# Optimization experiments

Hardware: AMD Instinct MI355X
Metric: run time of the kernel (lower is better)

The kernel has to match this reference:

```python
import jax, jax.numpy as jnp
import numpy as np

N = 20000      # nodes
E = 160000     # edges (avg degree 16)
IN_DIM = 256
HID = 128      # hidden_dim == per-head out_channels in PyG TransformerConv
HEADS = 4
EPS = 1e-5


def setup_inputs() -> dict:
    key = jax.random.key(0)
    ks = jax.random.split(key, 24)

    def w(k, shape, scale=0.05):
        return jax.random.normal(k, shape, dtype=jnp.float32) * scale

    inp = {
        "x": jax.random.normal(ks[0], (N, IN_DIM), dtype=jnp.float32),
        "edge_index": jax.random.randint(ks[1], (2, E), 0, N, dtype=jnp.int32),
        # input projection
        "lin_w": w(ks[2], (IN_DIM, HID)), "lin_b": jnp.zeros((HID,), jnp.float32),
    }
    i = 3
    for l in (1, 2):
        inp[f"q_w{l}"] = w(ks[i], (HID, HEADS * HID)); i += 1
        inp[f"q_b{l}"] = jnp.zeros((HEADS * HID,), jnp.float32)
        inp[f"k_w{l}"] = w(ks[i], (HID, HEADS * HID)); i += 1
        inp[f"k_b{l}"] = jnp.zeros((HEADS * HID,), jnp.float32)
        inp[f"v_w{l}"] = w(ks[i], (HID, HEADS * HID)); i += 1
        inp[f"v_b{l}"] = jnp.zeros((HEADS * HID,), jnp.float32)
        inp[f"s_w{l}"] = w(ks[i], (HID, HID)); i += 1
        inp[f"s_b{l}"] = jnp.zeros((HID,), jnp.float32)
        inp[f"ln_g{l}"] = jnp.ones((HID,), jnp.float32)
        inp[f"ln_b{l}"] = jnp.zeros((HID,), jnp.float32)
    return inp


def _segment_softmax(scores, seg, num):
    # scores: [E, HEADS], seg: [E] destination indices
    m = jax.ops.segment_max(scores, seg, num_segments=num)
    m = jnp.where(jnp.isfinite(m), m, 0.0)  # guard empty segments
    e = jnp.exp(scores - m[seg])
    d = jax.ops.segment_sum(e, seg, num_segments=num)
    return e / (d[seg] + 1e-16)


def _transformer_conv(x, src, dst, qw, qb, kw, kb, vw, vb, sw, sb):
    # PyG TransformerConv(HID, HID, heads=HEADS, concat=False)
    n = x.shape[0]
    q = (x @ qw + qb).reshape(n, HEADS, HID)
    k = (x @ kw + kb).reshape(n, HEADS, HID)
    v = (x @ vw + vb).reshape(n, HEADS, HID)
    # per-edge attention: query at dst (i), key/value at src (j)
    alpha = jnp.einsum("ehd,ehd->eh", q[dst], k[src]) / jnp.sqrt(jnp.float32(HID))
    alpha = _segment_softmax(alpha, dst, n)                 # [E, HEADS]
    msg = v[src] * alpha[..., None]                          # [E, HEADS, HID]
    out = jax.ops.segment_sum(msg, dst, num_segments=n)      # [N, HEADS, HID]
    out = out.mean(axis=1)                                   # concat=False -> head mean
    return out + x @ sw + sb                                 # root skip connection


def _layer_norm(x, g, b):
    mu = x.mean(-1, keepdims=True)
    var = ((x - mu) ** 2).mean(-1, keepdims=True)
    return (x - mu) * jax.lax.rsqrt(var + EPS) * g + b


def reference(x, edge_index, lin_w, lin_b,
              q_w1, q_b1, k_w1, k_b1, v_w1, v_b1, s_w1, s_b1, ln_g1, ln_b1,
              q_w2, q_b2, k_w2, k_b2, v_w2, v_b2, s_w2, s_b2, ln_g2, ln_b2):
    src, dst = edge_index[0], edge_index[1]
    h = jax.nn.relu(x @ lin_w + lin_b)
    h1 = _transformer_conv(h, src, dst, q_w1, q_b1, k_w1, k_b1, v_w1, v_b1, s_w1, s_b1)
    h = _layer_norm(h1 + h, ln_g1, ln_b1)
    h2 = _transformer_conv(h, src, dst, q_w2, q_b2, k_w2, k_b2, v_w2, v_b2, s_w2, s_b2)
    h = _layer_norm(h2 + h, ln_g2, ln_b2)
    return h
```

## Files before the change

### kernel.cpp

```cpp
#include <hip/hip_runtime.h>
#include <math.h>

#define NNODE 20000
#define NEDGE 160000
#define IN_DIMV 256
#define HIDV 128

typedef __attribute__((ext_vector_type(8))) short bf16x8;
typedef __attribute__((ext_vector_type(4))) float f32x4;
typedef __attribute__((ext_vector_type(2))) float f32x2;

__device__ __forceinline__ float bf2f(unsigned short u) {
    union { unsigned int i; float f; } x; x.i = ((unsigned int)u) << 16; return x.f;
}
__device__ __forceinline__ unsigned short f2bf(float f) {
    union { float f; unsigned int i; } x; x.f = f;
    unsigned int r = x.i + 0x7fffu + ((x.i >> 16) & 1u);
    return (unsigned short)(r >> 16);
}
__device__ __forceinline__ void unpack8(uint4 p, float* f) {
    f[0] = bf2f((unsigned short)(p.x & 0xffff)); f[1] = bf2f((unsigned short)(p.x >> 16));
    f[2] = bf2f((unsigned short)(p.y & 0xffff)); f[3] = bf2f((unsigned short)(p.y >> 16));
    f[4] = bf2f((unsigned short)(p.z & 0xffff)); f[5] = bf2f((unsigned short)(p.z >> 16));
    f[6] = bf2f((unsigned short)(p.w & 0xffff)); f[7] = bf2f((unsigned short)(p.w >> 16));
}
__device__ __forceinline__ void unpack8f8(uint2 p, float* f) {
    f32x2 a;
    a = __builtin_amdgcn_cvt_pk_f32_fp8((int)p.x, false); f[0] = a.x; f[1] = a.y;
    a = __builtin_amdgcn_cvt_pk_f32_fp8((int)p.x, true);  f[2] = a.x; f[3] = a.y;
    a = __builtin_amdgcn_cvt_pk_f32_fp8((int)p.y, false); f[4] = a.x; f[5] = a.y;
    a = __builtin_amdgcn_cvt_pk_f32_fp8((int)p.y, true);  f[6] = a.x; f[7] = a.y;
}
__device__ __forceinline__ unsigned char f2fp8(float v) {
    int pk = __builtin_amdgcn_cvt_pk_fp8_f32(v, v, 0, false);
    return (unsigned char)(pk & 0xff);
}
__device__ __forceinline__ void gld_lds16(const unsigned short* g, unsigned short* l) {
    __builtin_amdgcn_global_load_lds((const __attribute__((address_space(1))) void*)g,
                                     (__attribute__((address_space(3))) void*)l, 16, 0, 0);
}

__global__ void convert_kernel(
    const float* __restrict__ x, const float* __restrict__ lin_w,
    const float* __restrict__ qw0, const float* __restrict__ kw0,
    const float* __restrict__ vw0, const float* __restrict__ sw0,
    const float* __restrict__ qw1, const float* __restrict__ kw1,
    const float* __restrict__ vw1, const float* __restrict__ sw1,
    unsigned short* __restrict__ xbf, unsigned short* __restrict__ arena)
{
    int idx = blockIdx.x * 256 + threadIdx.x;
    if (idx < 5120000) { xbf[idx] = f2bf(x[idx]); return; }
    int id2 = idx - 5120000;
    if (id2 >= 458752) return;
    float v;
    if (id2 < 32768) {
        int n = id2 >> 8, k = id2 & 255;
        v = lin_w[k * 128 + n];
    } else {
        int t = id2 - 32768;
        int l = t / 212992, r = t % 212992;
        int n = r >> 7, k = r & 127;
        const float* qw = l ? qw1 : qw0;
        const float* kw = l ? kw1 : kw0;
        const float* vw = l ? vw1 : vw0;
        const float* sw = l ? sw1 : sw0;
        if (n < 1536) {
            const float* w = (n < 512) ? qw : (n < 1024) ? kw : vw;
            v = w[k * 512 + (n & 511)];
        } else {
            v = sw[k * 128 + (n - 1536)];
        }
    }
    arena[id2] = f2bf(v);
}

template <int MODE, int K>
__global__ __launch_bounds__(256) void mfma_gemm(
    const unsigned short* __restrict__ A, const unsigned short* __restrict__ WT,
    const float* __restrict__ b0, const float* __restrict__ b1,
    const float* __restrict__ b2, const float* __restrict__ b3,
    unsigned short* __restrict__ qb_out, unsigned char* __restrict__ kv8_out,
    float* __restrict__ pre_out, unsigned short* __restrict__ hbf_out)
{
    __shared__ unsigned short smem[8192];
    unsigned short* As = smem;
    unsigned short* Bs = smem + 4096;
    unsigned short* ot = smem;
    unsigned char* ot8 = (unsigned char*)smem;

    int tid = threadIdx.x;
    int lane = tid & 63;
    int w = tid >> 6;
    int wm = w & 1, wn = w >> 1;
    int bm = blockIdx.x * 128;
    int bn = blockIdx.y * 128;

    int srow = lane >> 2;
    int scol = (lane & 3) * 8;
    int ar0 = bm + w * 32 + srow;      if (ar0 > NNODE - 1) ar0 = NNODE - 1;
    int ar1 = bm + w * 32 + 16 + srow; if (ar1 > NNODE - 1) ar1 = NNODE - 1;
    int br0 = bn + w * 32 + srow;
    int br1 = bn + w * 32 + 16 + srow;

    f32x4 acc[4][4] = {};

    int arow = wm * 64 + (lane & 15);
    int brow = wn * 64 + (lane & 15);
    int koff = (lane >> 4) * 8;

    for (int k0 = 0; k0 < K; k0 += 32) {
        gld_lds16(A + (size_t)ar0 * K + k0 + scol, As + (w * 32) * 32);
        gld_lds16(A + (size_t)ar1 * K + k0 + scol, As + (w * 32 + 16) * 32);
        gld_lds16(WT + (size_t)br0 * K + k0 + scol, Bs + (w * 32) * 32);
        gld_lds16(WT + (size_t)br1 * K + k0 + scol, Bs + (w * 32 + 16) * 32);
        __syncthreads();
        bf16x8 fa[4], fb[4];
#pragma unroll
        for (int i = 0; i < 4; i++) fa[i] = *(const bf16x8*)&As[(arow + i * 16) * 32 + koff];
#pragma unroll
        for (int i = 0; i < 4; i++) fb[i] = *(const bf16x8*)&Bs[(brow + i * 16) * 32 + koff];
#pragma unroll
        for (int mi = 0; mi < 4; mi++)
#pragma unroll
            for (int ni = 0; ni < 4; ni++)
                acc[mi][ni] = __builtin_amdgcn_mfma_f32_16x16x32_bf16(fa[mi], fb[ni], acc[mi][ni], 0, 0, 0);
        __syncthreads();
    }

    int quad = lane >> 4, lcol = lane & 15;

    if (MODE == 1 && bn >= 1536) {
#pragma unroll
        for (int ni = 0; ni < 4; ni++) {
            int col = bn + wn * 64 + ni * 16 + lcol;
            float bias = b3[col - 1536];
#pragma unroll
            for (int mi = 0; mi < 4; mi++) {
                int rowb = bm + wm * 64 + mi * 16 + quad * 4;
#pragma unroll
                for (int reg = 0; reg < 4; reg++) {
                    int row = rowb + reg;
                    if (row >= NNODE) continue;
                    pre_out[(size_t)row * HIDV + (col - 1536)] = acc[mi][ni][reg] + bias;
                }
            }
        }
        return;
    }

    if (MODE == 1 && bn >= 512) {
        const float* bb = (bn < 1024) ? (b1 + bn - 512) : (b2 + bn - 1024);
        int coff = bn - 512;
#pragma unroll
        for (int hh = 0; hh < 2; hh++) {
            __syncthreads();
            if (wm == hh) {
#pragma unroll
                for (int mi = 0; mi < 4; mi++) {
#pragma unroll
                    for (int ni = 0; ni < 4; ni++) {
                        int lc = wn * 64 + ni * 16 + lcol;
                        float bias = bb[lc];
#pragma unroll
                        for (int reg = 0; reg < 4; reg++) {
                            int lr = mi * 16 + quad * 4 + reg;
                            ot8[lr * 128 + lc] = f2fp8(acc[mi][ni][reg] + bias);
                        }
                    }
                }
            }
            __syncthreads();
            int r = tid >> 2, ch = tid & 3;
            int row = bm + hh * 64 + r;
            if (row < NNODE) {
                uint4* dp = (uint4*)(kv8_out + (size_t)row * 1024 + coff + ch * 32);
                const uint4* sp = (const uint4*)(ot8 + r * 128 + ch * 32);
                dp[0] = sp[0];
                dp[1] = sp[1];
            }
        }
        return;
    }

    unsigned short* dst = (MODE == 0) ? hbf_out : qb_out;
    int dstride = (MODE == 0) ? HIDV : 512;
    const float* bb = (MODE == 0) ? b0 : (b0 + bn);

#pragma unroll
    for (int hh = 0; hh < 2; hh++) {
        __syncthreads();
        if (wm == hh) {
#pragma unroll
            for (int mi = 0; mi < 4; mi++) {
#pragma unroll
                for (int ni = 0; ni < 4; ni++) {
                    int lc = wn * 64 + ni * 16 + lcol;
                    float bias = bb[lc];
#pragma unroll
                    for (int reg = 0; reg < 4; reg++) {
                        float v = acc[mi][ni][reg] + bias;
                        if (MODE == 0) v = fmaxf(v, 0.f);
                        ot[(mi * 16 + quad * 4 + reg) * 128 + lc] = f2bf(v);
                    }
                }
            }
        }
        __syncthreads();
        int r = tid >> 2, ch = tid & 3;
        int row = bm + hh * 64 + r;
        if (row < NNODE) {
            uint4* dp = (uint4*)(dst + (size_t)row * dstride + (MODE == 0 ? 0 : bn) + ch * 32);
            const uint4* sp = (const uint4*)(ot + r * 128 + ch * 32);
#pragma unroll
            for (int q = 0; q < 4; q++) dp[q] = sp[q];
        }
    }
}

__global__ void hist_kernel(const int* __restrict__ ei, int* __restrict__ counts) {
    int e = blockIdx.x * blockDim.x + threadIdx.x;
    if (e < NEDGE) atomicAdd(&counts[ei[NEDGE + e]], 1);
}

__global__ __launch_bounds__(1024) void scan_kernel(int* __restrict__ cursor,
                                                    int* __restrict__ rowptr) {
    __shared__ int part[1024];
    int tid = threadIdx.x;
    const int CH = 20;
    int base = tid * CH;
    int loc[CH];
    int s = 0;
#pragma unroll
    for (int j = 0; j < CH; j++) {
        int idx = base + j;
        int c = (idx < NNODE) ? cursor[idx] : 0;
        loc[j] = s;
        s += c;
    }
    part[tid] = s;
    __syncthreads();
    for (int off = 1; off < 1024; off <<= 1) {
        int t = (tid >= off) ? part[tid - off] : 0;
        __syncthreads();
        part[tid] += t;
        __syncthreads();
    }
    int offs = part[tid] - s;
#pragma unroll
    for (int j = 0; j < CH; j++) {
        int idx = base + j;
        if (idx < NNODE) {
            int rv = offs + loc[j];
            rowptr[idx] = rv;
            cursor[idx] = rv;
        }
    }
    if (tid == 0) rowptr[NNODE] = NEDGE;
}

__global__ void scatter_kernel(const int* __restrict__ ei, int* __restrict__ cursor,
                               int* __restrict__ colsrc) {
    int e = blockIdx.x * blockDim.x + threadIdx.x;
    if (e < NEDGE) {
        int d = ei[NEDGE + e];
        int p = atomicAdd(&cursor[d], 1);
        colsrc[p] = ei[e];
    }
}

__global__ __launch_bounds__(256) void attn_ln_kernel(
    const unsigned short* __restrict__ qb, const unsigned char* __restrict__ kv8,
    const int* __restrict__ rowptr, const int* __restrict__ colsrc,
    const float* __restrict__ pre, const float* __restrict__ g,
    const float* __restrict__ b,
    unsigned short* __restrict__ hbf ,
    float* __restrict__ extout)
{
    int lane = threadIdx.x & 63;
    int wid = threadIdx.x >> 6;
    int i = blockIdx.x * 4 + wid;
    if (i >= NNODE) return;
    int rs = rowptr[i], re = rowptr[i + 1];
    int cnt = re - rs;

    float qr[8];
    {
        uint4 p = *(const uint4*)(qb + (size_t)i * 512 + lane * 8);
        unpack8(p, qr);
#pragma unroll
        for (int j = 0; j < 8; j++) qr[j] *= 0.0883883476483184f;
    }

    float m = -INFINITY, l = 0.f;
    float acc[8] = {0.f, 0.f, 0.f, 0.f, 0.f, 0.f, 0.f, 0.f};

    if (cnt > 0) {
        int nidx[4];
#pragma unroll
        for (int t = 0; t < 4; t++) nidx[t] = colsrc[rs + ((t < cnt) ? t : (cnt - 1))];
        uint2 kc[4], vc[4];
#pragma unroll
        for (int t = 0; t < 4; t++) {
            const unsigned char* r = kv8 + (size_t)nidx[t] * 1024 + lane * 8;
            kc[t] = *(const uint2*)r;
            vc[t] = *(const uint2*)(r + 512);
        }
#pragma unroll
        for (int t = 0; t < 4; t++) nidx[t] = (4 + t < cnt) ? colsrc[rs + 4 + t] : 0;

        for (int j0 = 0; j0 < cnt; j0 += 4) {
            uint2 kn[4], vn[4];
            bool more = (j0 + 4) < cnt;
            if (more) {
#pragma unroll
                for (int t = 0; t < 4; t++) {
                    const unsigned char* r = kv8 + (size_t)nidx[t] * 1024 + lane * 8;
                    kn[t] = *(const uint2*)r;
                    vn[t] = *(const uint2*)(r + 512);
                }
#pragma unroll
                for (int t = 0; t < 4; t++) nidx[t] = (j0 + 8 + t < cnt) ? colsrc[rs + j0 + 8 + t] : 0;
            }
            float d[4];
#pragma unroll
            for (int u = 0; u < 4; u++) {
                float kf[8];
                unpack8f8(kc[u], kf);
                d[u] = qr[0] * kf[0] + qr[1] * kf[1] + qr[2] * kf[2] + qr[3] * kf[3] +
                       qr[4] * kf[4] + qr[5] * kf[5] + qr[6] * kf[6] + qr[7] * kf[7];
            }
#pragma unroll
            for (int u = 0; u < 4; u++) d[u] += __shfl_xor(d[u], 8);
#pragma unroll
            for (int u = 0; u < 4; u++) d[u] += __shfl_xor(d[u], 4);
#pragma unroll
            for (int u = 0; u < 4; u++) d[u] += __shfl_xor(d[u], 2);
#pragma unroll
            for (int u = 0; u < 4; u++) d[u] += __shfl_xor(d[u], 1);
#pragma unroll
            for (int u = 0; u < 4; u++) if (j0 + u >= cnt) d[u] = -3.0e38f;
            float mq = fmaxf(fmaxf(d[0], d[1]), fmaxf(d[2], d[3]));
            float mn = fmaxf(m, mq);
            float scale = __expf(m - mn);
            float p0 = __expf(d[0] - mn), p1 = __expf(d[1] - mn);
            float p2 = __expf(d[2] - mn), p3 = __expf(d[3] - mn);
            l = l * scale + ((p0 + p1) + (p2 + p3));
            m = mn;
#pragma unroll
            for (int c = 0; c < 8; c++) acc[c] *= scale;
            float pp[4] = {p0, p1, p2, p3};
#pragma unroll
            for (int u = 0; u < 4; u++) {
                float vf[8];
                unpack8f8(vc[u], vf);
                float pu = pp[u];
#pragma unroll
                for (int c = 0; c < 8; c++) acc[c] += pu * vf[c];
            }
            if (more) {
#pragma unroll
                for (int t = 0; t < 4; t++) { kc[t] = kn[t]; vc[t] = vn[t]; }
            }
        }
    }

    float linv = 0.25f / (l + 1e-16f);
#pragma unroll
    for (int c = 0; c < 8; c++) acc[c] *= linv;
#pragma unroll
    for (int c = 0; c < 8; c++) {
        acc[c] += __shfl_xor(acc[c], 16);
        acc[c] += __shfl_xor(acc[c], 32);
    }

    int c16 = lane & 15;
    size_t base = (size_t)i * HIDV + c16 * 8;
    float4 p0r = ((const float4*)(pre + base))[0];
    float4 p1r = ((const float4*)(pre + base))[1];
    float hv[8];
    unpack8(*(const uint4*)(hbf + base), hv);
    float vals[8];
    vals[0] = acc[0] + p0r.x + hv[0]; vals[1] = acc[1] + p0r.y + hv[1];
    vals[2] = acc[2] + p0r.z + hv[2]; vals[3] = acc[3] + p0r.w + hv[3];
    vals[4] = acc[4] + p1r.x + hv[4]; vals[5] = acc[5] + p1r.y + hv[5];
    vals[6] = acc[6] + p1r.z + hv[6]; vals[7] = acc[7] + p1r.w + hv[7];

    float s = 0.f;
#pragma unroll
    for (int c = 0; c < 8; c++) s += vals[c];
    s += __shfl_xor(s, 1); s += __shfl_xor(s, 2);
    s += __shfl_xor(s, 4); s += __shfl_xor(s, 8);
    float mu = s * (1.f / 128.f);
    float vs = 0.f;
#pragma unroll
    for (int c = 0; c < 8; c++) { float dx = vals[c] - mu; vs += dx * dx; }
    vs += __shfl_xor(vs, 1); vs += __shfl_xor(vs, 2);
    vs += __shfl_xor(vs, 4); vs += __shfl_xor(vs, 8);
    float rstd = rsqrtf(vs * (1.f / 128.f) + 1e-5f);

    float4 g0 = ((const float4*)(g + c16 * 8))[0];
    float4 g1 = ((const float4*)(g + c16 * 8))[1];
    float4 bb0 = ((const float4*)(b + c16 * 8))[0];
    float4 bb1 = ((const float4*)(b + c16 * 8))[1];
    float y[8];
    y[0] = (vals[0] - mu) * rstd * g0.x + bb0.x; y[1] = (vals[1] - mu) * rstd * g0.y + bb0.y;
    y[2] = (vals[2] - mu) * rstd * g0.z + bb0.z; y[3] = (vals[3] - mu) * rstd * g0.w + bb0.w;
    y[4] = (vals[4] - mu) * rstd * g1.x + bb1.x; y[5] = (vals[5] - mu) * rstd * g1.y + bb1.y;
    y[6] = (vals[6] - mu) * rstd * g1.z + bb1.z; y[7] = (vals[7] - mu) * rstd * g1.w + bb1.w;

    if (lane < 16) {
        unsigned short tmp[8] = {f2bf(y[0]), f2bf(y[1]), f2bf(y[2]), f2bf(y[3]),
                                 f2bf(y[4]), f2bf(y[5]), f2bf(y[6]), f2bf(y[7])};
        *(uint4*)(hbf + base) = *(uint4*)tmp;
        if (extout) {
            ((float4*)(extout + base))[0] = make_float4(y[0], y[1], y[2], y[3]);
            ((float4*)(extout + base))[1] = make_float4(y[4], y[5], y[6], y[7]);
        }
    }
}

extern "C" void kernel_launch(void* const* d_in, const int* in_sizes, int n_in,
                              void* d_out, int out_size, void* d_ws, size_t ws_size,
                              hipStream_t stream) {
    const float* x = (const float*)d_in[0];
    const int* ei = (const int*)d_in[1];

    char* ws = (char*)d_ws;
    unsigned short* hbf = (unsigned short*)(ws + 0);
    float* pre = (float*)(ws + 5120000);
    unsigned short* qb = (unsigned short*)(ws + 15360000);
    unsigned char* kv8 = (unsigned char*)(ws + 35840000);
    unsigned short* xbf = (unsigned short*)(ws + 56320000);
    int* rowptr = (int*)(ws + 66560000);
    int* cursor = (int*)(ws + 66640064);
    int* colsrc = (int*)(ws + 66720064);
    unsigned short* arena = (unsigned short*)(ws + 67360064);

    convert_kernel<<<21793, 256, 0, stream>>>(
        x, (const float*)d_in[2],
        (const float*)d_in[4], (const float*)d_in[6], (const float*)d_in[8], (const float*)d_in[10],
        (const float*)d_in[14], (const float*)d_in[16], (const float*)d_in[18], (const float*)d_in[20],
        xbf, arena);

    hipMemsetAsync(cursor, 0, NNODE * sizeof(int), stream);
    hist_kernel<<<(NEDGE + 255) / 256, 256, 0, stream>>>(ei, cursor);
    scan_kernel<<<1, 1024, 0, stream>>>(cursor, rowptr);
    scatter_kernel<<<(NEDGE + 255) / 256, 256, 0, stream>>>(ei, cursor, colsrc);

    const int GM = (NNODE + 127) / 128;

    mfma_gemm<0, 256><<<dim3(GM, 1), 256, 0, stream>>>(
        xbf, arena, (const float*)d_in[3], nullptr, nullptr, nullptr,
        nullptr, nullptr, nullptr, hbf);

    for (int l = 0; l < 2; l++) {
        int o = 4 + l * 10;
        const unsigned short* WT = arena + 32768 + l * 212992;
        mfma_gemm<1, 128><<<dim3(GM, 13), 256, 0, stream>>>(
            hbf, WT,
            (const float*)d_in[o + 1], (const float*)d_in[o + 3],
            (const float*)d_in[o + 5], (const float*)d_in[o + 7],
            qb, kv8, pre, nullptr);

        attn_ln_kernel<<<(NNODE + 3) / 4, 256, 0, stream>>>(
            qb, kv8, rowptr, colsrc, pre,
            (const float*)d_in[o + 8], (const float*)d_in[o + 9],
            hbf, (l == 1) ? (float*)d_out : nullptr);
    }
}
```

Before: 325.2 us.

## Process two nodes per wavefront in attention and load full K tile in GEMM

The attention+LayerNorm kernel now maps each node to a 32-lane half-wavefront, so each wave handles two nodes. Each lane loads 16-byte fp8 K/V chunks instead of 8-byte chunks, and the edge pipeline prefetches two neighbours instead of four. In the K=128 GEMM, the whole K dimension is staged into a larger LDS buffer with a single barrier instead of one barrier per k-step. The aim is wider memory accesses, fewer idle lanes and less synchronisation. The cost is more registers and LDS, which may lower occupancy, and the bounds check assumes N is divisible by 8.

```diff
diff --git a/kernel.cpp b/kernel.cpp
--- a/kernel.cpp
+++ b/kernel.cpp
@@ -24,12 +24,16 @@
     f[4] = bf2f((unsigned short)(p.z & 0xffff)); f[5] = bf2f((unsigned short)(p.z >> 16));
     f[6] = bf2f((unsigned short)(p.w & 0xffff)); f[7] = bf2f((unsigned short)(p.w >> 16));
 }
-__device__ __forceinline__ void unpack8f8(uint2 p, float* f) {
-    f32x2 a;
-    a = __builtin_amdgcn_cvt_pk_f32_fp8((int)p.x, false); f[0] = a.x; f[1] = a.y;
-    a = __builtin_amdgcn_cvt_pk_f32_fp8((int)p.x, true);  f[2] = a.x; f[3] = a.y;
-    a = __builtin_amdgcn_cvt_pk_f32_fp8((int)p.y, false); f[4] = a.x; f[5] = a.y;
-    a = __builtin_amdgcn_cvt_pk_f32_fp8((int)p.y, true);  f[6] = a.x; f[7] = a.y;
+__device__ __forceinline__ void unpack8f8_w(unsigned int a, unsigned int b, float* f) {
+    f32x2 t;
+    t = __builtin_amdgcn_cvt_pk_f32_fp8((int)a, false); f[0] = t.x; f[1] = t.y;
+    t = __builtin_amdgcn_cvt_pk_f32_fp8((int)a, true);  f[2] = t.x; f[3] = t.y;
+    t = __builtin_amdgcn_cvt_pk_f32_fp8((int)b, false); f[4] = t.x; f[5] = t.y;
+    t = __builtin_amdgcn_cvt_pk_f32_fp8((int)b, true);  f[6] = t.x; f[7] = t.y;
+}
+__device__ __forceinline__ void unpack16f8(uint4 p, float* f) {
+    unpack8f8_w(p.x, p.y, f);
+    unpack8f8_w(p.z, p.w, f + 8);
 }
 __device__ __forceinline__ unsigned char f2fp8(float v) {
     int pk = __builtin_amdgcn_cvt_pk_fp8_f32(v, v, 0, false);
@@ -82,9 +86,8 @@
     unsigned short* __restrict__ qb_out, unsigned char* __restrict__ kv8_out,
     float* __restrict__ pre_out, unsigned short* __restrict__ hbf_out)
 {
-    __shared__ unsigned short smem[8192];
-    unsigned short* As = smem;
-    unsigned short* Bs = smem + 4096;
+    constexpr bool FULLK = (K == 128);
+    __shared__ unsigned short smem[FULLK ? 32768 : 8192];
     unsigned short* ot = smem;
     unsigned char* ot8 = (unsigned char*)smem;
 
@@ -103,28 +106,56 @@
     int br1 = bn + w * 32 + 16 + srow;
 
     f32x4 acc[4][4] = {};
-
     int arow = wm * 64 + (lane & 15);
     int brow = wn * 64 + (lane & 15);
     int koff = (lane >> 4) * 8;
 
-    for (int k0 = 0; k0 < K; k0 += 32) {
-        gld_lds16(A + (size_t)ar0 * K + k0 + scol, As + (w * 32) * 32);
-        gld_lds16(A + (size_t)ar1 * K + k0 + scol, As + (w * 32 + 16) * 32);
-        gld_lds16(WT + (size_t)br0 * K + k0 + scol, Bs + (w * 32) * 32);
-        gld_lds16(WT + (size_t)br1 * K + k0 + scol, Bs + (w * 32 + 16) * 32);
+    if constexpr (FULLK) {
+        unsigned short* As = smem;
+        unsigned short* Bs = smem + 16384;
+#pragma unroll
+        for (int c = 0; c < 4; c++) {
+            int k0 = c * 32;
+            gld_lds16(A + (size_t)ar0 * K + k0 + scol, As + c * 4096 + (w * 32) * 32);
+            gld_lds16(A + (size_t)ar1 * K + k0 + scol, As + c * 4096 + (w * 32 + 16) * 32);
+            gld_lds16(WT + (size_t)br0 * K + k0 + scol, Bs + c * 4096 + (w * 32) * 32);
+            gld_lds16(WT + (size_t)br1 * K + k0 + scol, Bs + c * 4096 + (w * 32 + 16) * 32);
+        }
         __syncthreads();
-        bf16x8 fa[4], fb[4];
-#pragma unroll
-        for (int i = 0; i < 4; i++) fa[i] = *(const bf16x8*)&As[(arow + i * 16) * 32 + koff];
-#pragma unroll
-        for (int i = 0; i < 4; i++) fb[i] = *(const bf16x8*)&Bs[(brow + i * 16) * 32 + koff];
-#pragma unroll
-        for (int mi = 0; mi < 4; mi++)
-#pragma unroll
-            for (int ni = 0; ni < 4; ni++)
-                acc[mi][ni] = __builtin_amdgcn_mfma_f32_16x16x32_bf16(fa[mi], fb[ni], acc[mi][ni], 0, 0, 0);
-        __syncthreads();
+#pragma unroll
+        for (int c = 0; c < 4; c++) {
+            bf16x8 fa[4], fb[4];
+#pragma unroll
+            for (int i = 0; i < 4; i++) fa[i] = *(const bf16x8*)&As[c * 4096 + (arow + i * 16) * 32 + koff];
+#pragma unroll
+            for (int i = 0; i < 4; i++) fb[i] = *(const bf16x8*)&Bs[c * 4096 + (brow + i * 16) * 32 + koff];
+#pragma unroll
+            for (int mi = 0; mi < 4; mi++)
+#pragma unroll
+                for (int ni = 0; ni < 4; ni++)
+                    acc[mi][ni] = __builtin_amdgcn_mfma_f32_16x16x32_bf16(fa[mi], fb[ni], acc[mi][ni], 0, 0, 0);
+        }
+    } else {
+        unsigned short* As = smem;
+        unsigned short* Bs = smem + 4096;
+        for (int k0 = 0; k0 < K; k0 += 32) {
+            gld_lds16(A + (size_t)ar0 * K + k0 + scol, As + (w * 32) * 32);
+            gld_lds16(A + (size_t)ar1 * K + k0 + scol, As + (w * 32 + 16) * 32);
+            gld_lds16(WT + (size_t)br0 * K + k0 + scol, Bs + (w * 32) * 32);
+            gld_lds16(WT + (size_t)br1 * K + k0 + scol, Bs + (w * 32 + 16) * 32);
+            __syncthreads();
+            bf16x8 fa[4], fb[4];
+#pragma unroll
+            for (int i = 0; i < 4; i++) fa[i] = *(const bf16x8*)&As[(arow + i * 16) * 32 + koff];
+#pragma unroll
+            for (int i = 0; i < 4; i++) fb[i] = *(const bf16x8*)&Bs[(brow + i * 16) * 32 + koff];
+#pragma unroll
+            for (int mi = 0; mi < 4; mi++)
+#pragma unroll
+                for (int ni = 0; ni < 4; ni++)
+                    acc[mi][ni] = __builtin_amdgcn_mfma_f32_16x16x32_bf16(fa[mi], fb[ni], acc[mi][ni], 0, 0, 0);
+            __syncthreads();
+        }
     }
 
     int quad = lane >> 4, lcol = lane & 15;
@@ -278,143 +309,144 @@
 {
     int lane = threadIdx.x & 63;
     int wid = threadIdx.x >> 6;
-    int i = blockIdx.x * 4 + wid;
-    if (i >= NNODE) return;
+    int half = lane >> 5;
+    int sub = lane & 31;
+    int i = blockIdx.x * 8 + wid * 2 + half;
     int rs = rowptr[i], re = rowptr[i + 1];
     int cnt = re - rs;
 
-    float qr[8];
+    float qr[16];
     {
-        uint4 p = *(const uint4*)(qb + (size_t)i * 512 + lane * 8);
-        unpack8(p, qr);
-#pragma unroll
-        for (int j = 0; j < 8; j++) qr[j] *= 0.0883883476483184f;
+        const unsigned short* qp = qb + (size_t)i * 512 + sub * 16;
+        unpack8(*(const uint4*)qp, qr);
+        unpack8(*(const uint4*)(qp + 8), qr + 8);
+#pragma unroll
+        for (int j = 0; j < 16; j++) qr[j] *= 0.0883883476483184f;
     }
 
     float m = -INFINITY, l = 0.f;
-    float acc[8] = {0.f, 0.f, 0.f, 0.f, 0.f, 0.f, 0.f, 0.f};
+    float acc[16];
+#pragma unroll
+    for (int c = 0; c < 16; c++) acc[c] = 0.f;
 
     if (cnt > 0) {
-        int nidx[4];
-#pragma unroll
-        for (int t = 0; t < 4; t++) nidx[t] = colsrc[rs + ((t < cnt) ? t : (cnt - 1))];
-        uint2 kc[4], vc[4];
-#pragma unroll
-        for (int t = 0; t < 4; t++) {
-            const unsigned char* r = kv8 + (size_t)nidx[t] * 1024 + lane * 8;
-            kc[t] = *(const uint2*)r;
-            vc[t] = *(const uint2*)(r + 512);
-        }
-#pragma unroll
-        for (int t = 0; t < 4; t++) nidx[t] = (4 + t < cnt) ? colsrc[rs + 4 + t] : 0;
-
-        for (int j0 = 0; j0 < cnt; j0 += 4) {
-            uint2 kn[4], vn[4];
-            bool more = (j0 + 4) < cnt;
+        int nidx[2];
+        uint4 kc[2], vc[2];
+#pragma unroll
+        for (int t = 0; t < 2; t++) {
+            int s = colsrc[rs + ((t < cnt) ? t : (cnt - 1))];
+            const unsigned char* r = kv8 + (size_t)s * 1024 + sub * 16;
+            kc[t] = *(const uint4*)r;
+            vc[t] = *(const uint4*)(r + 512);
+            nidx[t] = (2 + t < cnt) ? colsrc[rs + 2 + t] : 0;
+        }
+
+        for (int j0 = 0; j0 < cnt; j0 += 2) {
+            uint4 kn[2], vn[2];
+            bool more = (j0 + 2) < cnt;
             if (more) {
 #pragma unroll
-                for (int t = 0; t < 4; t++) {
-                    const unsigned char* r = kv8 + (size_t)nidx[t] * 1024 + lane * 8;
-                    kn[t] = *(const uint2*)r;
-                    vn[t] = *(const uint2*)(r + 512);
+                for (int t = 0; t < 2; t++) {
+                    const unsigned char* r = kv8 + (size_t)nidx[t] * 1024 + sub * 16;
+                    kn[t] = *(const uint4*)r;
+                    vn[t] = *(const uint4*)(r + 512);
+                    nidx[t] = (j0 + 4 + t < cnt) ? colsrc[rs + j0 + 4 + t] : 0;
                 }
-#pragma unroll
-                for (int t = 0; t < 4; t++) nidx[t] = (j0 + 8 + t < cnt) ? colsrc[rs + j0 + 8 + t] : 0;
-            }
-            float d[4];
-#pragma unroll
-            for (int u = 0; u < 4; u++) {
-                float kf[8];
-                unpack8f8(kc[u], kf);
-                d[u] = qr[0] * kf[0] + qr[1] * kf[1] + qr[2] * kf[2] + qr[3] * kf[3] +
-                       qr[4] * kf[4] + qr[5] * kf[5] + qr[6] * kf[6] + qr[7] * kf[7];
-            }
-#pragma unroll
-            for (int u = 0; u < 4; u++) d[u] += __shfl_xor(d[u], 8);
-#pragma unroll
-            for (int u = 0; u < 4; u++) d[u] += __shfl_xor(d[u], 4);
-#pragma unroll
-            for (int u = 0; u < 4; u++) d[u] += __shfl_xor(d[u], 2);
-#pragma unroll
-            for (int u = 0; u < 4; u++) d[u] += __shfl_xor(d[u], 1);
-#pragma unroll
-            for (int u = 0; u < 4; u++) if (j0 + u >= cnt) d[u] = -3.0e38f;
-            float mq = fmaxf(fmaxf(d[0], d[1]), fmaxf(d[2], d[3]));
+            }
+            float d[2];
+#pragma unroll
+            for (int u = 0; u < 2; u++) {
+                float kf[16];
+                unpack16f8(kc[u], kf);
+                float s0 = 0.f;
+#pragma unroll
+                for (int c = 0; c < 16; c++) s0 += qr[c] * kf[c];
+                d[u] = s0;
+            }
+#pragma unroll
+            for (int u = 0; u < 2; u++) d[u] += __shfl_xor(d[u], 4);
+#pragma unroll
+            for (int u = 0; u < 2; u++) d[u] += __shfl_xor(d[u], 2);
+#pragma unroll
+            for (int u = 0; u < 2; u++) d[u] += __shfl_xor(d[u], 1);
+            if (j0 + 1 >= cnt) d[1] = -3.0e38f;
+            float mq = fmaxf(d[0], d[1]);
             float mn = fmaxf(m, mq);
             float scale = __expf(m - mn);
             float p0 = __expf(d[0] - mn), p1 = __expf(d[1] - mn);
-            float p2 = __expf(d[2] - mn), p3 = __expf(d[3] - mn);
-            l = l * scale + ((p0 + p1) + (p2 + p3));
+            l = l * scale + (p0 + p1);
             m = mn;
-#pragma unroll
-            for (int c = 0; c < 8; c++) acc[c] *= scale;
-            float pp[4] = {p0, p1, p2, p3};
-#pragma unroll
-            for (int u = 0; u < 4; u++) {
-                float vf[8];
-                unpack8f8(vc[u], vf);
-                float pu = pp[u];
-#pragma unroll
-                for (int c = 0; c < 8; c++) acc[c] += pu * vf[c];
-            }
+            float vf0[16], vf1[16];
+            unpack16f8(vc[0], vf0);
+            unpack16f8(vc[1], vf1);
+#pragma unroll
+            for (int c = 0; c < 16; c++) acc[c] = acc[c] * scale + p0 * vf0[c] + p1 * vf1[c];
             if (more) {
 #pragma unroll
-                for (int t = 0; t < 4; t++) { kc[t] = kn[t]; vc[t] = vn[t]; }
+                for (int t = 0; t < 2; t++) { kc[t] = kn[t]; vc[t] = vn[t]; }
             }
         }
     }
 
     float linv = 0.25f / (l + 1e-16f);
 #pragma unroll
-    for (int c = 0; c < 8; c++) acc[c] *= linv;
-#pragma unroll
-    for (int c = 0; c < 8; c++) {
+    for (int c = 0; c < 16; c++) acc[c] *= linv;
+#pragma unroll
+    for (int c = 0; c < 16; c++) {
+        acc[c] += __shfl_xor(acc[c], 8);
         acc[c] += __shfl_xor(acc[c], 16);
-        acc[c] += __shfl_xor(acc[c], 32);
-    }
-
-    int c16 = lane & 15;
-    size_t base = (size_t)i * HIDV + c16 * 8;
-    float4 p0r = ((const float4*)(pre + base))[0];
-    float4 p1r = ((const float4*)(pre + base))[1];
-    float hv[8];
-    unpack8(*(const uint4*)(hbf + base), hv);
-    float vals[8];
-    vals[0] = acc[0] + p0r.x + hv[0]; vals[1] = acc[1] + p0r.y + hv[1];
-    vals[2] = acc[2] + p0r.z + hv[2]; vals[3] = acc[3] + p0r.w + hv[3];
-    vals[4] = acc[4] + p1r.x + hv[4]; vals[5] = acc[5] + p1r.y + hv[5];
-    vals[6] = acc[6] + p1r.z + hv[6]; vals[7] = acc[7] + p1r.w + hv[7];
+    }
+
+    int cg = sub & 7;
+    size_t base = (size_t)i * HIDV + cg * 16;
+    float4 pr[4];
+#pragma unroll
+    for (int q = 0; q < 4; q++) pr[q] = ((const float4*)(pre + base))[q];
+    float hv[16];
+    unpack8(((const uint4*)(hbf + base))[0], hv);
+    unpack8(((const uint4*)(hbf + base))[1], hv + 8);
+    float vals[16];
+#pragma unroll
+    for (int q = 0; q < 4; q++) {
+        vals[q * 4 + 0] = acc[q * 4 + 0] + pr[q].x + hv[q * 4 + 0];
+        vals[q * 4 + 1] = acc[q * 4 + 1] + pr[q].y + hv[q * 4 + 1];
+        vals[q * 4 + 2] = acc[q * 4 + 2] + pr[q].z + hv[q * 4 + 2];
+        vals[q * 4 + 3] = acc[q * 4 + 3] + pr[q].w + hv[q * 4 + 3];
+    }
 
     float s = 0.f;
 #pragma unroll
-    for (int c = 0; c < 8; c++) s += vals[c];
-    s += __shfl_xor(s, 1); s += __shfl_xor(s, 2);
-    s += __shfl_xor(s, 4); s += __shfl_xor(s, 8);
+    for (int c = 0; c < 16; c++) s += vals[c];
+    s += __shfl_xor(s, 1); s += __shfl_xor(s, 2); s += __shfl_xor(s, 4);
     float mu = s * (1.f / 128.f);
     float vs = 0.f;
 #pragma unroll
-    for (int c = 0; c < 8; c++) { float dx = vals[c] - mu; vs += dx * dx; }
-    vs += __shfl_xor(vs, 1); vs += __shfl_xor(vs, 2);
-    vs += __shfl_xor(vs, 4); vs += __shfl_xor(vs, 8);
+    for (int c = 0; c < 16; c++) { float dx = vals[c] - mu; vs += dx * dx; }
+    vs += __shfl_xor(vs, 1); vs += __shfl_xor(vs, 2); vs += __shfl_xor(vs, 4);
     float rstd = rsqrtf(vs * (1.f / 128.f) + 1e-5f);
 
-    float4 g0 = ((const float4*)(g + c16 * 8))[0];
-    float4 g1 = ((const float4*)(g + c16 * 8))[1];
-    float4 bb0 = ((const float4*)(b + c16 * 8))[0];
-    float4 bb1 = ((const float4*)(b + c16 * 8))[1];
-    float y[8];
-    y[0] = (vals[0] - mu) * rstd * g0.x + bb0.x; y[1] = (vals[1] - mu) * rstd * g0.y + bb0.y;
-    y[2] = (vals[2] - mu) * rstd * g0.z + bb0.z; y[3] = (vals[3] - mu) * rstd * g0.w + bb0.w;
-    y[4] = (vals[4] - mu) * rstd * g1.x + bb1.x; y[5] = (vals[5] - mu) * rstd * g1.y + bb1.y;
-    y[6] = (vals[6] - mu) * rstd * g1.z + bb1.z; y[7] = (vals[7] - mu) * rstd * g1.w + bb1.w;
-
-    if (lane < 16) {
-        unsigned short tmp[8] = {f2bf(y[0]), f2bf(y[1]), f2bf(y[2]), f2bf(y[3]),
-                                 f2bf(y[4]), f2bf(y[5]), f2bf(y[6]), f2bf(y[7])};
-        *(uint4*)(hbf + base) = *(uint4*)tmp;
+    float gv[16], bv[16];
+#pragma unroll
+    for (int q = 0; q < 4; q++) {
+        float4 gg = ((const float4*)(g + cg * 16))[q];
+        float4 bb = ((const float4*)(b + cg * 16))[q];
+        gv[q * 4 + 0] = gg.x; gv[q * 4 + 1] = gg.y; gv[q * 4 + 2] = gg.z; gv[q * 4 + 3] = gg.w;
+        bv[q * 4 + 0] = bb.x; bv[q * 4 + 1] = bb.y; bv[q * 4 + 2] = bb.z; bv[q * 4 + 3] = bb.w;
+    }
+    float y[16];
+#pragma unroll
+    for (int c = 0; c < 16; c++) y[c] = (vals[c] - mu) * rstd * gv[c] + bv[c];
+
+    if (sub < 8) {
+        unsigned short tmp[16];
+#pragma unroll
+        for (int c = 0; c < 16; c++) tmp[c] = f2bf(y[c]);
+        ((uint4*)(hbf + base))[0] = ((uint4*)tmp)[0];
+        ((uint4*)(hbf + base))[1] = ((uint4*)tmp)[1];
         if (extout) {
-            ((float4*)(extout + base))[0] = make_float4(y[0], y[1], y[2], y[3]);
-            ((float4*)(extout + base))[1] = make_float4(y[4], y[5], y[6], y[7]);
+#pragma unroll
+            for (int q = 0; q < 4; q++)
+                ((float4*)(extout + base))[q] = make_float4(y[q * 4 + 0], y[q * 4 + 1], y[q * 4 + 2], y[q * 4 + 3]);
         }
     }
 }
@@ -462,7 +494,7 @@
             (const float*)d_in[o + 5], (const float*)d_in[o + 7],
             qb, kv8, pre, nullptr);
 
-        attn_ln_kernel<<<(NNODE + 3) / 4, 256, 0, stream>>>(
+        attn_ln_kernel<<<NNODE / 8, 256, 0, stream>>>(
             qb, kv8, rowptr, colsrc, pre,
             (const float*)d_in[o + 8], (const float*)d_in[o + 9],
             hbf, (l == 1) ? (float*)d_out : nullptr);
```

Result: no change. 323.5 us (-0.5%).
